# Performance work log

Hardware: AMD Instinct MI355X
Metric: run time of the kernel (lower is better)

Reference implementation:

```python
import jax, jax.numpy as jnp
import numpy as np

B, L, D, N = 4, 1024, 1024, 16
HD = D // N
DFF = 4 * D
EPS = 1e-5


def _ln(x, g, b):
    m = jnp.mean(x, axis=-1, keepdims=True)
    v = jnp.mean(jnp.square(x - m), axis=-1, keepdims=True)
    return (x - m) * jax.lax.rsqrt(v + EPS) * g + b


def setup_inputs() -> dict:
    key = jax.random.key(0)
    ks = jax.random.split(key, 8)
    s = 0.02
    return {
        "x": jax.random.normal(ks[0], (B, L, D), jnp.float32),
        "decay": jax.random.uniform(ks[1], (N, L, L), jnp.float32),
        "ln1_g": jnp.ones((D,), jnp.float32),
        "ln1_b": jnp.zeros((D,), jnp.float32),
        "proj_W": jax.random.normal(ks[2], (4 * D, D), jnp.float32) * s,
        "proj_b": jnp.zeros((4 * D,), jnp.float32),
        "reto_W": jax.random.normal(ks[3], (D, D), jnp.float32) * s,
        "reto_b": jnp.zeros((D,), jnp.float32),
        "ln2_g": jnp.ones((D,), jnp.float32),
        "ln2_b": jnp.zeros((D,), jnp.float32),
        "ffn1_W": jax.random.normal(ks[4], (DFF, D), jnp.float32) * s,
        "ffn1_b": jnp.zeros((DFF,), jnp.float32),
        "ffn2_W": jax.random.normal(ks[5], (D, DFF), jnp.float32) * s,
        "ffn2_b": jnp.zeros((D,), jnp.float32),
    }


def reference(x, decay, ln1_g, ln1_b, proj_W, proj_b, reto_W, reto_b,
              ln2_g, ln2_b, ffn1_W, ffn1_b, ffn2_W, ffn2_b):
    ln_x = _ln(x, ln1_g, ln1_b)
    p = ln_x @ proj_W.T + proj_b                      # [B, L, 4D]
    q, k, v, xo = jnp.split(p, 4, axis=-1)            # each [B, L, D]

    def heads(t):  # [B, L, D] -> [B, N, L, HD]
        return t.reshape(B, L, N, HD).transpose(0, 2, 1, 3)

    q, k, v = heads(q), heads(k), heads(v)
    scores = jnp.einsum('bnld,bnmd->bnlm', q, k) * decay[None]  # [B,N,L,L]
    ret = jnp.einsum('bnlm,bnmd->bnld', scores, v)              # [B,N,L,HD]
    ret = ret.transpose(0, 2, 1, 3).reshape(B, L, D)
    ret = ret * jax.nn.silu(xo)                                  # gated
    ret = ret @ reto_W.T + reto_b
    x = x + ret
    h = _ln(x, ln2_g, ln2_b)
    h = jax.nn.gelu(h @ ffn1_W.T + ffn1_b, approximate=False) @ ffn2_W.T + ffn2_b
    return x + h
```

## Files before the change

### kernel.cpp

```cpp
#include <hip/hip_runtime.h>


typedef _Float16 f16;
typedef _Float16 f16x8 __attribute__((ext_vector_type(8)));
typedef float floatx4 __attribute__((ext_vector_type(4)));

#define EP_BIAS_F16      0
#define EP_DECAY_F16     1
#define EP_BIAS_GELU_F16 2
#define EP_PARTIAL_F32   3

template <bool F32> struct out_sel { typedef f16 T; };
template <> struct out_sel<true>   { typedef float T; };

__device__ __forceinline__ void gload_lds16(const void* g, void* s) {
    __builtin_amdgcn_global_load_lds(
        (const __attribute__((address_space(1))) unsigned int*)g,
        (__attribute__((address_space(3))) unsigned int*)s, 16, 0, 0);
}

__device__ __forceinline__ float erf_fast(float x) {
    const float ax = fabsf(x);
    const float t  = __builtin_amdgcn_rcpf(1.f + 0.3275911f * ax);
    const float p  = t * (0.254829592f + t * (-0.284496736f + t * (1.421413741f +
                     t * (-1.453152027f + t * 1.061405429f))));
    const float r  = 1.f - p * __expf(-ax * ax);
    return copysignf(r, x);
}

__global__ __launch_bounds__(256, 2) void attn_fused(
    const f16* __restrict__ p, const f16* __restrict__ vT,
    const float* __restrict__ decay, f16* __restrict__ gated)
{
    const int y  = blockIdx.y;
    const int bp = y >> 4, h = y & 15;
    const int m0 = blockIdx.x * 64;

    __shared__ __align__(16) f16 Kb[2][64 * 64];
    __shared__ __align__(16) f16 Vb[2][64 * 64];
    __shared__ __align__(16) f16 Ss[4][16 * 68];

    const int t    = threadIdx.x;
    const int lane = t & 63;
    const int w    = t >> 6;
    const int quad = lane >> 4;
    const int fr   = lane & 15;
    const int wq0  = w * 16;

    const int b0 = bp * 2, b1 = b0 + 1;
    const f16*   Qg0 = p + (size_t)(b0 * 1024 + m0) * 4096 + h * 64;
    const f16*   Qg1 = p + (size_t)(b1 * 1024 + m0) * 4096 + h * 64;
    const f16*   Kg0 = p + (size_t)(b0 * 1024) * 4096 + 1024 + h * 64;
    const f16*   Kg1 = p + (size_t)(b1 * 1024) * 4096 + 1024 + h * 64;
    const f16*   Vg0 = vT + (size_t)(b0 * 16 + h) * 65536;
    const f16*   Vg1 = vT + (size_t)(b1 * 16 + h) * 65536;
    const f16*   XOg0 = p + (size_t)(b0 * 1024 + m0) * 4096 + 3072 + h * 64;
    const f16*   XOg1 = p + (size_t)(b1 * 1024 + m0) * 4096 + 3072 + h * 64;
    const float* Dg  = decay + (size_t)h * 1048576 + (size_t)m0 * 1024;

    f16x8 q00, q01, q10, q11;
    {
        const size_t qrow = (size_t)(wq0 + fr) * 4096;
        q00 = *(const f16x8*)(Qg0 + qrow + (0 * 4 + quad) * 8);
        q01 = *(const f16x8*)(Qg0 + qrow + (1 * 4 + quad) * 8);
        q10 = *(const f16x8*)(Qg1 + qrow + (0 * 4 + quad) * 8);
        q11 = *(const f16x8*)(Qg1 + qrow + (1 * 4 + quad) * 8);
    }

    floatx4 oa0[4] = {}, oa1[4] = {};
    float dA[16], dB[16];

    const float* Dt = Dg + (size_t)(wq0 + quad * 4) * 1024 + fr;

#define DLOAD(dst, jj) { _Pragma("unroll") \
    for (int tn = 0; tn < 4; ++tn) { _Pragma("unroll") \
      for (int r = 0; r < 4; ++r) \
        dst[tn * 4 + r] = Dt[(size_t)r * 1024 + (jj) + tn * 16]; } }

#define STAGE(Kgp, Vgp, jj, pb) { _Pragma("unroll") \
    for (int i = 0; i < 2; ++i) { \
      const int ci = t + i * 256; \
      const int r  = ci >> 3; \
      const int c  = ((ci & 7) ^ (r & 7)) * 8; \
      gload_lds16((Kgp) + (size_t)((jj) + r) * 4096 + c, &Kb[pb][ci * 8]); \
      gload_lds16((Vgp) + (size_t)r * 1024 + (jj) + c, &Vb[pb][ci * 8]); \
    } }

#define STEP(qa, qb, oa, dreg, pb) { \
    floatx4 sa[4] = {}; \
    _Pragma("unroll") \
    for (int kc = 0; kc < 2; ++kc) { \
      const int cc = kc * 4 + quad; \
      f16x8 bf[4]; \
      _Pragma("unroll") \
      for (int tn = 0; tn < 4; ++tn) { \
        const int kv = tn * 16 + fr; \
        bf[tn] = *(const f16x8*)&Kb[pb][(kv * 8 + (cc ^ (kv & 7))) * 8]; \
      } \
      _Pragma("unroll") \
      for (int tn = 0; tn < 4; ++tn) \
        sa[tn] = __builtin_amdgcn_mfma_f32_16x16x32_f16(kc ? (qb) : (qa), bf[tn], sa[tn], 0, 0, 0); \
    } \
    _Pragma("unroll") \
    for (int tn = 0; tn < 4; ++tn) { _Pragma("unroll") \
      for (int r = 0; r < 4; ++r) \
        Ss[w][(quad * 4 + r) * 68 + tn * 16 + fr] = (f16)(sa[tn][r] * dreg[tn * 4 + r]); } \
    _Pragma("unroll") \
    for (int kc = 0; kc < 2; ++kc) { \
      const int cc = kc * 4 + quad; \
      const f16x8 af = *(const f16x8*)&Ss[w][fr * 68 + cc * 8]; \
      f16x8 bf[4]; \
      _Pragma("unroll") \
      for (int tn = 0; tn < 4; ++tn) { \
        const int d = tn * 16 + fr; \
        bf[tn] = *(const f16x8*)&Vb[pb][(d * 8 + (cc ^ (d & 7))) * 8]; \
      } \
      _Pragma("unroll") \
      for (int tn = 0; tn < 4; ++tn) \
        oa[tn] = __builtin_amdgcn_mfma_f32_16x16x32_f16(af, bf[tn], oa[tn], 0, 0, 0); \
    } }

#define EPILOG(oa, XOgp, bq) { \
    _Pragma("unroll") \
    for (int tn = 0; tn < 4; ++tn) { _Pragma("unroll") \
      for (int r = 0; r < 4; ++r) { \
        const int qrow = wq0 + quad * 4 + r; \
        const int d = tn * 16 + fr; \
        float g = (float)XOgp[(size_t)qrow * 4096 + d]; \
        g = g * __builtin_amdgcn_rcpf(1.f + __expf(-g)); \
        Ss[w][(quad * 4 + r) * 68 + tn * 16 + fr] = (f16)(oa[tn][r] * g); \
      } } \
    f16* Og = gated + (size_t)((bq) * 1024 + m0 + wq0) * 1024 + h * 64; \
    _Pragma("unroll") \
    for (int i = 0; i < 2; ++i) { \
      const int jj = lane + i * 64; \
      const int rr = jj >> 3; \
      const int cc = jj & 7; \
      const uint2 lo = *(const uint2*)&Ss[w][rr * 68 + cc * 8]; \
      const uint2 hi = *(const uint2*)&Ss[w][rr * 68 + cc * 8 + 4]; \
      uint4 val = make_uint4(lo.x, lo.y, hi.x, hi.y); \
      *(uint4*)(Og + (size_t)rr * 1024 + cc * 8) = val; \
    } }

    STAGE(Kg0, Vg0, 0, 0);
    DLOAD(dA, 0);
    __syncthreads();

    for (int tt = 0; tt < 16; tt += 2) {
        const int j0 = tt << 6;
        STAGE(Kg1, Vg1, j0, 1);
        STEP(q00, q01, oa0, dA, 0);
        __syncthreads();
        STAGE(Kg0, Vg0, j0 + 64, 0);
        DLOAD(dB, j0 + 64);
        STEP(q10, q11, oa1, dA, 1);
        __syncthreads();
        STAGE(Kg1, Vg1, j0 + 64, 1);
        STEP(q00, q01, oa0, dB, 0);
        __syncthreads();
        if (tt < 14) {
            STAGE(Kg0, Vg0, j0 + 128, 0);
            DLOAD(dA, j0 + 128);
        }
        STEP(q10, q11, oa1, dB, 1);
        __syncthreads();
    }

    EPILOG(oa0, XOg0, b0);
    EPILOG(oa1, XOg1, b1);

#undef DLOAD
#undef STAGE
#undef STEP
#undef EPILOG
}

template <int BM, int BN, int WM, int WN, int EP>
__global__ __launch_bounds__(256, 4) void gemm_bt(
    const f16* __restrict__ A, const f16* __restrict__ B, void* __restrict__ Cv,
    int M, int N, int K, int lda, int ldb, int ldc,
    long long sAo, long long sAi, long long sBo, long long sBi,
    long long sCo, long long sCi, int inner,
    int nsplit, int Kc, long long sCk,
    const float* __restrict__ bias,
    const void* __restrict__ aux, long long sXo, long long sXi, int ldaux)
{
    constexpr bool OUT_F32 = (EP == EP_PARTIAL_F32);
    typedef typename out_sel<OUT_F32>::T OutT;
    constexpr int ESIZE       = OUT_F32 ? 4 : 2;
    constexpr int CSTRIDE     = BN + 4;
    constexpr int TILE_BYTES  = (BM + BN) * 64 * 2;
    constexpr int STAGE_BYTES = BM * CSTRIDE * ESIZE;
    constexpr int SMEM_BYTES  = TILE_BYTES > STAGE_BYTES ? TILE_BYTES : STAGE_BYTES;

    __shared__ __align__(16) char smem[SMEM_BYTES];
    f16*  As = (f16*)smem;
    f16*  Bs = (f16*)(smem + BM * 128);
    OutT* Cs = (OutT*)smem;

    int z = blockIdx.z;
    const int ks = z % nsplit; z /= nsplit;
    const int zo = z / inner, zi = z % inner;
    A += zo * sAo + zi * sAi;
    B += zo * sBo + zi * sBi;
    const long long cOff = (long long)zo * sCo + (long long)zi * sCi + (long long)ks * sCk;
    const long long xOff = (long long)zo * sXo + (long long)zi * sXi;

    const int m0 = blockIdx.y * BM;
    const int n0 = blockIdx.x * BN;

    const int t    = threadIdx.x;
    const int lane = t & 63;
    const int w    = t >> 6;
    const int wm   = (w >> 1) * (WM * 16);
    const int wn   = (w & 1) * (WN * 16);
    const int fr   = lane & 15;
    const int quad = lane >> 4;

    constexpr int ACH = BM / 32;
    constexpr int BCH = BN / 32;

    floatx4 acc[WM][WN] = {};

    const int kbeg = ks * Kc, kend = kbeg + Kc;
    for (int kk = kbeg; kk < kend; kk += 64) {
#pragma unroll
        for (int i = 0; i < ACH; ++i) {
            const int ci = t + i * 256;
            const int r  = ci >> 3;
            const int c  = ((ci & 7) ^ (r & 7)) * 8;
            gload_lds16(A + (size_t)(m0 + r) * lda + kk + c, &As[ci * 8]);
        }
#pragma unroll
        for (int i = 0; i < BCH; ++i) {
            const int ci = t + i * 256;
            const int r  = ci >> 3;
            const int c  = ((ci & 7) ^ (r & 7)) * 8;
            gload_lds16(B + (size_t)(n0 + r) * ldb + kk + c, &Bs[ci * 8]);
        }
        __syncthreads();

#pragma unroll
        for (int kh = 0; kh < 2; ++kh) {
            const int cc = kh * 4 + quad;
            f16x8 af[WM], bf[WN];
#pragma unroll
            for (int tm = 0; tm < WM; ++tm) {
                const int r = wm + tm * 16 + fr;
                af[tm] = *(const f16x8*)&As[(r * 8 + (cc ^ (r & 7))) * 8];
            }
#pragma unroll
            for (int tn = 0; tn < WN; ++tn) {
                const int r = wn + tn * 16 + fr;
                bf[tn] = *(const f16x8*)&Bs[(r * 8 + (cc ^ (r & 7))) * 8];
            }
#pragma unroll
            for (int tm = 0; tm < WM; ++tm)
#pragma unroll
                for (int tn = 0; tn < WN; ++tn)
                    acc[tm][tn] = __builtin_amdgcn_mfma_f32_16x16x32_f16(af[tm], bf[tn], acc[tm][tn], 0, 0, 0);
        }
        __syncthreads();
    }

    const int er = quad * 4;
    const int ec = lane & 15;
#pragma unroll
    for (int tm = 0; tm < WM; ++tm) {
#pragma unroll
        for (int tn = 0; tn < WN; ++tn) {
#pragma unroll
            for (int r = 0; r < 4; ++r) {
                const int lrow = wm + tm * 16 + er + r;
                const int col  = wn + tn * 16 + ec;
                const int grow = m0 + lrow;
                const int gcol = n0 + col;
                const float v = acc[tm][tn][r];
                float val;
                if constexpr (EP == EP_BIAS_F16) {
                    val = v + bias[gcol];
                } else if constexpr (EP == EP_DECAY_F16) {
                    const float* dk = (const float*)aux + xOff;
                    val = v * dk[(size_t)grow * ldaux + gcol];
                } else if constexpr (EP == EP_BIAS_GELU_F16) {
                    const float u = v + bias[gcol];
                    val = 0.5f * u * (1.f + erf_fast(u * 0.70710678118f));
                } else {
                    val = v;
                }
                Cs[lrow * CSTRIDE + col] = (OutT)val;
            }
        }
    }
    __syncthreads();

    constexpr int PER_ROW = BN * ESIZE / 16;
    constexpr int NCHUNK  = (BM * PER_ROW) / 256;
#pragma unroll
    for (int i = 0; i < NCHUNK; ++i) {
        const int j  = t + i * 256;
        const int rr = j / PER_ROW;
        const int cc = j - rr * PER_ROW;
        const char* src = smem + (size_t)rr * (CSTRIDE * ESIZE) + (size_t)cc * 16;
        uint4 val;
        if constexpr (OUT_F32) {
            val = *(const uint4*)src;
        } else {
            const uint2 lo = *(const uint2*)src;
            const uint2 hi = *(const uint2*)(src + 8);
            val = make_uint4(lo.x, lo.y, hi.x, hi.y);
        }
        char* dst = (char*)Cv +
            (size_t)(cOff + (long long)(m0 + rr) * ldc + n0) * ESIZE +
            (size_t)cc * 16;
        *(uint4*)dst = val;
    }
}

__global__ __launch_bounds__(256) void reduce2_bias_res(
    const float4* __restrict__ P, const float* __restrict__ bias,
    const float4* __restrict__ res, float4* __restrict__ out)
{
    const int i = blockIdx.x * 256 + threadIdx.x;
    const int col4 = i & 255;
    const float4 a = P[i];
    const float4 b = P[i + 1048576];
    const float4 r = res[i];
    const float4 bi = ((const float4*)bias)[col4];
    float4 o;
    o.x = a.x + b.x + r.x + bi.x;
    o.y = a.y + b.y + r.y + bi.y;
    o.z = a.z + b.z + r.z + bi.z;
    o.w = a.w + b.w + r.w + bi.w;
    out[i] = o;
}

__global__ __launch_bounds__(256) void ln_to_f16(
    const float* __restrict__ x, const float* __restrict__ g,
    const float* __restrict__ b, f16* __restrict__ out)
{
    const int row = blockIdx.x;
    const int t = threadIdx.x;
    const float4 xv = ((const float4*)(x + (size_t)row * 1024))[t];
    float s  = xv.x + xv.y + xv.z + xv.w;
    float ss = xv.x * xv.x + xv.y * xv.y + xv.z * xv.z + xv.w * xv.w;
    for (int o = 32; o > 0; o >>= 1) {
        s  += __shfl_down(s, o, 64);
        ss += __shfl_down(ss, o, 64);
    }
    __shared__ float red[8];
    const int wv = t >> 6;
    if ((t & 63) == 0) { red[wv] = s; red[wv + 4] = ss; }
    __syncthreads();
    s  = red[0] + red[1] + red[2] + red[3];
    ss = red[4] + red[5] + red[6] + red[7];
    const float mean = s * (1.f / 1024.f);
    const float var  = ss * (1.f / 1024.f) - mean * mean;
    const float rstd = rsqrtf(var + 1e-5f);
    const float4 gv = ((const float4*)g)[t];
    const float4 bv = ((const float4*)b)[t];
    alignas(8) f16 h[4];
    h[0] = (f16)((xv.x - mean) * rstd * gv.x + bv.x);
    h[1] = (f16)((xv.y - mean) * rstd * gv.y + bv.y);
    h[2] = (f16)((xv.z - mean) * rstd * gv.z + bv.z);
    h[3] = (f16)((xv.w - mean) * rstd * gv.w + bv.w);
    ((uint2*)(out + (size_t)row * 1024))[t] = *(uint2*)h;
}

__global__ __launch_bounds__(256) void cast_f32_f16(
    const float* __restrict__ in, f16* __restrict__ out, int n4)
{
    const int i = blockIdx.x * 256 + threadIdx.x;
    if (i < n4) {
        const float4 v = ((const float4*)in)[i];
        alignas(8) f16 h[4] = {(f16)v.x, (f16)v.y, (f16)v.z, (f16)v.w};
        ((uint2*)out)[i] = *(uint2*)h;
    }
}

__global__ __launch_bounds__(256) void transpose_v(
    const f16* __restrict__ p, f16* __restrict__ vT)
{
    const int z = blockIdx.y;
    const int b = z >> 4, h = z & 15;
    const int m0 = blockIdx.x * 64;
    __shared__ f16 tile[64][72];
    const int t = threadIdx.x;
    const f16* src = p + (size_t)(b * 1024 + m0) * 4096 + 2048 + h * 64;
#pragma unroll
    for (int pass = 0; pass < 4; ++pass) {
        const int r = (t >> 4) + pass * 16;
        const int c = (t & 15) * 4;
        *(uint2*)&tile[r][c] = *(const uint2*)(src + (size_t)r * 4096 + c);
    }
    __syncthreads();
    f16* dst = vT + (size_t)z * 65536 + m0;
#pragma unroll
    for (int pass = 0; pass < 4; ++pass) {
        const int d  = (t >> 4) + pass * 16;
        const int mc = (t & 15) * 4;
        alignas(8) f16 tmp[4] = {tile[mc][d], tile[mc + 1][d], tile[mc + 2][d], tile[mc + 3][d]};
        *(uint2*)(dst + (size_t)d * 1024 + mc) = *(uint2*)tmp;
    }
}

extern "C" void kernel_launch(void* const* d_in, const int* in_sizes, int n_in,
                              void* d_out, int out_size, void* d_ws, size_t ws_size,
                              hipStream_t stream) {
    const float* x      = (const float*)d_in[0];
    const float* decay  = (const float*)d_in[1];
    const float* ln1_g  = (const float*)d_in[2];
    const float* ln1_b  = (const float*)d_in[3];
    const float* proj_W = (const float*)d_in[4];
    const float* proj_b = (const float*)d_in[5];
    const float* reto_W = (const float*)d_in[6];
    const float* reto_b = (const float*)d_in[7];
    const float* ln2_g  = (const float*)d_in[8];
    const float* ln2_b  = (const float*)d_in[9];
    const float* ffn1_W = (const float*)d_in[10];
    const float* ffn1_b = (const float*)d_in[11];
    const float* ffn2_W = (const float*)d_in[12];
    const float* ffn2_b = (const float*)d_in[13];
    float* out = (float*)d_out;

    char* w = (char*)d_ws;
    auto alloc = [&](size_t bytes) { char* r = w; w += (bytes + 255) & ~(size_t)255; return r; };
    f16*   Wp   = (f16*)alloc((size_t)4096 * 1024 * 2);
    f16*   Wr   = (f16*)alloc((size_t)1024 * 1024 * 2);
    f16*   W1   = (f16*)alloc((size_t)4096 * 1024 * 2);
    f16*   W2   = (f16*)alloc((size_t)1024 * 4096 * 2);
    f16*   buf8 = (f16*)alloc((size_t)4096 * 1024 * 2);
    f16*   p    = (f16*)alloc((size_t)4096 * 4096 * 2);
    f16*   S    = (f16*)alloc((size_t)16 * 1024 * 1024 * 2);
    float* y    = (float*)alloc((size_t)4096 * 1024 * 4);

    f16*   lnx   = buf8;
    f16*   vT    = buf8;
    f16*   hln   = buf8;
    f16*   gated = Wp;
    f16*   ffh   = p;
    float* Pk    = (float*)S;

    cast_f32_f16<<<4096, 256, 0, stream>>>(proj_W, Wp, 1048576);
    cast_f32_f16<<<1024, 256, 0, stream>>>(reto_W, Wr, 262144);
    cast_f32_f16<<<4096, 256, 0, stream>>>(ffn1_W, W1, 1048576);
    cast_f32_f16<<<4096, 256, 0, stream>>>(ffn2_W, W2, 1048576);

    ln_to_f16<<<4096, 256, 0, stream>>>(x, ln1_g, ln1_b, lnx);

    gemm_bt<128, 128, 4, 4, EP_BIAS_F16><<<dim3(32, 32, 1), 256, 0, stream>>>(
        lnx, Wp, p, 4096, 4096, 1024, 1024, 1024, 4096,
        0, 0, 0, 0, 0, 0, 1, 1, 1024, 0, proj_b, nullptr, 0, 0, 0);

    transpose_v<<<dim3(16, 64), 256, 0, stream>>>(p, vT);

    attn_fused<<<dim3(16, 32), 256, 0, stream>>>(p, vT, decay, gated);

    gemm_bt<128, 64, 4, 2, EP_PARTIAL_F32><<<dim3(16, 32, 2), 256, 0, stream>>>(
        gated, Wr, Pk, 4096, 1024, 1024, 1024, 1024, 1024,
        0, 0, 0, 0, 0, 0, 1, 2, 512, 4194304, nullptr, nullptr, 0, 0, 0);
    reduce2_bias_res<<<4096, 256, 0, stream>>>(
        (const float4*)Pk, reto_b, (const float4*)x, (float4*)y);

    ln_to_f16<<<4096, 256, 0, stream>>>(y, ln2_g, ln2_b, hln);

    gemm_bt<128, 128, 4, 4, EP_BIAS_GELU_F16><<<dim3(32, 32, 1), 256, 0, stream>>>(
        hln, W1, ffh, 4096, 4096, 1024, 1024, 1024, 4096,
        0, 0, 0, 0, 0, 0, 1, 1, 1024, 0, ffn1_b, nullptr, 0, 0, 0);

    gemm_bt<128, 64, 4, 2, EP_PARTIAL_F32><<<dim3(16, 32, 2), 256, 0, stream>>>(
        ffh, W2, Pk, 4096, 1024, 4096, 4096, 4096, 1024,
        0, 0, 0, 0, 0, 0, 1, 2, 2048, 4194304, nullptr, nullptr, 0, 0, 0);
    reduce2_bias_res<<<4096, 256, 0, stream>>>(
        (const float4*)Pk, ffn2_b, (const float4*)y, (float4*)out);
}
```

Baseline: 410.4 us.

## Use 128x128 tiles, XCD block swizzle and direct stores for split-K GEMMs

The two split-K fp32-partial GEMMs (retention output projection and FFN2) move from 128x64 to 128x128 tiles, halving the grid in x. A block-index remap spreads consecutive blocks across the eight XCDs. The fp32 epilogue now writes accumulators straight to global memory instead of staging through LDS, which lowers the LDS footprint and drops a barrier. In exchange there are fewer blocks (512), which may reduce occupancy, and the direct stores are less coalesced.

```diff
diff --git a/kernel.cpp b/kernel.cpp
--- a/kernel.cpp
+++ b/kernel.cpp
@@ -175,7 +175,7 @@
 #undef EPILOG
 }
 
-template <int BM, int BN, int WM, int WN, int EP>
+template <int BM, int BN, int WM, int WN, int EP, int XSWZ>
 __global__ __launch_bounds__(256, 4) void gemm_bt(
     const f16* __restrict__ A, const f16* __restrict__ B, void* __restrict__ Cv,
     int M, int N, int K, int lda, int ldb, int ldc,
@@ -190,7 +190,7 @@
     constexpr int ESIZE       = OUT_F32 ? 4 : 2;
     constexpr int CSTRIDE     = BN + 4;
     constexpr int TILE_BYTES  = (BM + BN) * 64 * 2;
-    constexpr int STAGE_BYTES = BM * CSTRIDE * ESIZE;
+    constexpr int STAGE_BYTES = OUT_F32 ? 0 : BM * CSTRIDE * ESIZE;
     constexpr int SMEM_BYTES  = TILE_BYTES > STAGE_BYTES ? TILE_BYTES : STAGE_BYTES;
 
     __shared__ __align__(16) char smem[SMEM_BYTES];
@@ -206,8 +206,17 @@
     const long long cOff = (long long)zo * sCo + (long long)zi * sCi + (long long)ks * sCk;
     const long long xOff = (long long)zo * sXo + (long long)zi * sXi;
 
-    const int m0 = blockIdx.y * BM;
-    const int n0 = blockIdx.x * BN;
+    int bx = blockIdx.x, by = blockIdx.y;
+    if constexpr (XSWZ) {
+        const int gx  = gridDim.x;
+        const int nb  = gx * gridDim.y;
+        const int lin = bx + gx * by;
+        const int nlin = (lin & 7) * (nb >> 3) + (lin >> 3);
+        bx = nlin % gx;
+        by = nlin / gx;
+    }
+    const int m0 = by * BM;
+    const int n0 = bx * BN;
 
     const int t    = threadIdx.x;
     const int lane = t & 63;
@@ -265,6 +274,21 @@
 
     const int er = quad * 4;
     const int ec = lane & 15;
+    if constexpr (OUT_F32) {
+        float* Pg = (float*)Cv + cOff;
+#pragma unroll
+        for (int tm = 0; tm < WM; ++tm)
+#pragma unroll
+            for (int tn = 0; tn < WN; ++tn)
+#pragma unroll
+                for (int r = 0; r < 4; ++r) {
+                    const int grow = m0 + wm + tm * 16 + er + r;
+                    const int gcol = n0 + wn + tn * 16 + ec;
+                    Pg[(size_t)grow * ldc + gcol] = acc[tm][tn][r];
+                }
+        return;
+    }
+
 #pragma unroll
     for (int tm = 0; tm < WM; ++tm) {
 #pragma unroll
@@ -302,14 +326,9 @@
         const int rr = j / PER_ROW;
         const int cc = j - rr * PER_ROW;
         const char* src = smem + (size_t)rr * (CSTRIDE * ESIZE) + (size_t)cc * 16;
-        uint4 val;
-        if constexpr (OUT_F32) {
-            val = *(const uint4*)src;
-        } else {
-            const uint2 lo = *(const uint2*)src;
-            const uint2 hi = *(const uint2*)(src + 8);
-            val = make_uint4(lo.x, lo.y, hi.x, hi.y);
-        }
+        const uint2 lo = *(const uint2*)src;
+        const uint2 hi = *(const uint2*)(src + 8);
+        uint4 val = make_uint4(lo.x, lo.y, hi.x, hi.y);
         char* dst = (char*)Cv +
             (size_t)(cOff + (long long)(m0 + rr) * ldc + n0) * ESIZE +
             (size_t)cc * 16;
@@ -448,7 +467,7 @@
 
     ln_to_f16<<<4096, 256, 0, stream>>>(x, ln1_g, ln1_b, lnx);
 
-    gemm_bt<128, 128, 4, 4, EP_BIAS_F16><<<dim3(32, 32, 1), 256, 0, stream>>>(
+    gemm_bt<128, 128, 4, 4, EP_BIAS_F16, 0><<<dim3(32, 32, 1), 256, 0, stream>>>(
         lnx, Wp, p, 4096, 4096, 1024, 1024, 1024, 4096,
         0, 0, 0, 0, 0, 0, 1, 1, 1024, 0, proj_b, nullptr, 0, 0, 0);
 
@@ -456,7 +475,7 @@
 
     attn_fused<<<dim3(16, 32), 256, 0, stream>>>(p, vT, decay, gated);
 
-    gemm_bt<128, 64, 4, 2, EP_PARTIAL_F32><<<dim3(16, 32, 2), 256, 0, stream>>>(
+    gemm_bt<128, 128, 4, 4, EP_PARTIAL_F32, 1><<<dim3(8, 32, 2), 256, 0, stream>>>(
         gated, Wr, Pk, 4096, 1024, 1024, 1024, 1024, 1024,
         0, 0, 0, 0, 0, 0, 1, 2, 512, 4194304, nullptr, nullptr, 0, 0, 0);
     reduce2_bias_res<<<4096, 256, 0, stream>>>(
@@ -464,11 +483,11 @@
 
     ln_to_f16<<<4096, 256, 0, stream>>>(y, ln2_g, ln2_b, hln);
 
-    gemm_bt<128, 128, 4, 4, EP_BIAS_GELU_F16><<<dim3(32, 32, 1), 256, 0, stream>>>(
+    gemm_bt<128, 128, 4, 4, EP_BIAS_GELU_F16, 0><<<dim3(32, 32, 1), 256, 0, stream>>>(
         hln, W1, ffh, 4096, 4096, 1024, 1024, 1024, 4096,
         0, 0, 0, 0, 0, 0, 1, 1, 1024, 0, ffn1_b, nullptr, 0, 0, 0);
 
-    gemm_bt<128, 64, 4, 2, EP_PARTIAL_F32><<<dim3(16, 32, 2), 256, 0, stream>>>(
+    gemm_bt<128, 128, 4, 4, EP_PARTIAL_F32, 1><<<dim3(8, 32, 2), 256, 0, stream>>>(
         ffh, W2, Pk, 4096, 1024, 4096, 4096, 4096, 1024,
         0, 0, 0, 0, 0, 0, 1, 2, 2048, 4194304, nullptr, nullptr, 0, 0, 0);
     reduce2_bias_res<<<4096, 256, 0, stream>>>(
```

Result: faster. 399.7 us (-2.6%).
